# Kernel optimization log

Hardware: AMD Instinct MI355X
Metric: run time of the kernel (lower is better)

The kernel has to match this reference:

```python
import jax, jax.numpy as jnp
import numpy as np

B, N, C = 4, 4096, 1024          # batch, seq_len (input_size), channels
H, D = 16, 64                    # nhead, dim_d (per-head dim)
K_DIM = 256                      # dim_k (Linformer compression)
FF = 4096                        # dim_ff
L = 2                            # depth
EPS = 1e-5


def setup_inputs() -> dict:
    key = jax.random.key(0)
    ks = jax.random.split(key, 16)
    s_qkv = 1.0 / np.sqrt(C)
    s_e = np.sqrt(2.0 / N)        # kaiming_normal fan_in relu
    s_wo = 1.0 / np.sqrt(H * D)
    s_f1 = 1.0 / np.sqrt(C)
    s_f2 = 1.0 / np.sqrt(FF)
    return {
        "x": jax.random.normal(ks[0], (B, N, C), jnp.float32),
        # shared E/F projection (layerwise parameter sharing => one Linear)
        "E_w": jax.random.normal(ks[1], (K_DIM, N), jnp.float32) * s_e,
        "E_b": jax.random.uniform(ks[2], (K_DIM,), jnp.float32, -s_e, s_e),
        # per-layer stacked per-head Q/K/V weights (bias=False)
        "Wq": jax.random.uniform(ks[3], (L, H, D, C), jnp.float32, -s_qkv, s_qkv),
        "Wk": jax.random.uniform(ks[4], (L, H, D, C), jnp.float32, -s_qkv, s_qkv),
        "Wv": jax.random.uniform(ks[5], (L, H, D, C), jnp.float32, -s_qkv, s_qkv),
        "wo_w": jax.random.uniform(ks[6], (L, C, H * D), jnp.float32, -s_wo, s_wo),
        "wo_b": jax.random.uniform(ks[7], (L, C), jnp.float32, -s_wo, s_wo),
        "ln1_g": jnp.ones((L, C), jnp.float32),
        "ln1_b": jnp.zeros((L, C), jnp.float32),
        "ff_w1": jax.random.uniform(ks[8], (L, FF, C), jnp.float32, -s_f1, s_f1),
        "ff_b1": jax.random.uniform(ks[9], (L, FF), jnp.float32, -s_f1, s_f1),
        "ff_w2": jax.random.uniform(ks[10], (L, C, FF), jnp.float32, -s_f2, s_f2),
        "ff_b2": jax.random.uniform(ks[11], (L, C), jnp.float32, -s_f2, s_f2),
        "ln2_g": jnp.ones((L, C), jnp.float32),
        "ln2_b": jnp.zeros((L, C), jnp.float32),
    }


def _layernorm(t, g, b):
    m = jnp.mean(t, axis=-1, keepdims=True)
    v = jnp.var(t, axis=-1, keepdims=True)
    return (t - m) * jax.lax.rsqrt(v + EPS) * g + b


def reference(x, E_w, E_b, Wq, Wk, Wv, wo_w, wo_b, ln1_g, ln1_b,
              ff_w1, ff_b1, ff_w2, ff_b2, ln2_g, ln2_b):
    scale = 1.0 / jnp.sqrt(jnp.float32(D))
    for l in range(Wq.shape[0]):
        # per-head projections, all heads batched: [B,H,N,D]
        Q = jnp.einsum('bnc,hdc->bhnd', x, Wq[l])
        K = jnp.einsum('bnc,hdc->bhnd', x, Wk[l])
        V = jnp.einsum('bnc,hdc->bhnd', x, Wv[l])
        # E-projection of K^T along seq axis: [B,H,D,K_DIM]
        KE = jnp.einsum('bhnd,kn->bhdk', K, E_w) + E_b
        # scores + softmax: [B,H,N,K_DIM]
        P = jax.nn.softmax(jnp.einsum('bhnd,bhdk->bhnk', Q, KE) * scale, axis=-1)
        # F-projection of V (F shares weights with E layerwise): [B,H,K_DIM,D]
        VF = jnp.einsum('bhnd,kn->bhkd', V, E_w) + E_b[:, None]
        attn = jnp.einsum('bhnk,bhkd->bhnd', P, VF)
        # concat heads in head order -> [B,N,H*D]
        cat = jnp.swapaxes(attn, 1, 2).reshape(x.shape[0], x.shape[1], -1)
        out = cat @ wo_w[l].T + wo_b[l]
        x = _layernorm(x + out, ln1_g[l], ln1_b[l])
        # feed-forward (relu)
        h = jax.nn.relu(x @ ff_w1[l].T + ff_b1[l])
        ff = h @ ff_w2[l].T + ff_b2[l]
        x = _layernorm(x + ff, ln2_g[l], ln2_b[l])
    return x
```

## Files before the change

### kernel.cpp

```cpp
#include <hip/hip_runtime.h>
#include <hip/hip_bf16.h>

typedef __attribute__((ext_vector_type(8))) short short8;
typedef __attribute__((ext_vector_type(4))) float f32x4;

__device__ __forceinline__ unsigned short dev_f2bf(float f) {
  __hip_bfloat16 b = __float2bfloat16(f);
  union { __hip_bfloat16 b; unsigned short u; } c; c.b = b; return c.u;
}
__device__ __forceinline__ float dev_bf2f(unsigned short u) {
  union { unsigned int i; float f; } c; c.i = ((unsigned int)u) << 16; return c.f;
}

__device__ __forceinline__ void gload_lds16(const unsigned short* g, unsigned short* l) {
  __builtin_amdgcn_global_load_lds(
      (const __attribute__((address_space(1))) void*)(const void*)g,
      (__attribute__((address_space(3))) void*)(void*)l, 16, 0, 0);
}

struct GemmP {
  const unsigned short* A;
  const unsigned short* B;
  void* C;
  const float* biasN;
  const float* biasM;
  long long aHi, aLo, bHi, bLo, cHi, cLo;
  int K;
  int sAm;
  int sBn;
  int sCm, sCn;
  float scale;
  int relu;
  int cdtype;
};

__global__ __launch_bounds__(512, 2) void gemm256(GemmP p) {
  __shared__ __align__(16) unsigned short lds[2][2][256 * 64];

  const int tid = threadIdx.x;
  const int lane = tid & 63;
  const int wid = tid >> 6;
  const int wm = wid >> 2;
  const int wn = wid & 3;

  int id = blockIdx.y * gridDim.x + blockIdx.x;
  const int nwg = gridDim.x * gridDim.y;
  if ((nwg & 7) == 0) id = (id & 7) * (nwg >> 3) + (id >> 3);
  const long long m0 = (long long)(id / gridDim.y) * 256;
  const long long n0 = (long long)(id % gridDim.y) * 256;

  const int srow8 = lane >> 3;
  const int scol = ((lane & 7) ^ srow8) * 8;

  f32x4 acc[8][4];
#pragma unroll
  for (int i = 0; i < 8; i++)
#pragma unroll
    for (int j = 0; j < 4; j++)
      acc[i][j] = f32x4{0.f, 0.f, 0.f, 0.f};

  const int nt = p.K >> 6;

  auto stage = [&](int buf, int t) {
    const long long k0 = (long long)t * 64;
#pragma unroll
    for (int h = 0; h < 4; h++)
      gload_lds16(p.A + (m0 + h * 64 + wid * 8 + srow8) * p.sAm + k0 + scol,
                  &lds[buf][0][(h * 64 + wid * 8) * 64]);
#pragma unroll
    for (int h = 0; h < 4; h++)
      gload_lds16(p.B + (n0 + h * 64 + wid * 8 + srow8) * p.sBn + k0 + scol,
                  &lds[buf][1][(h * 64 + wid * 8) * 64]);
  };

  stage(0, 0);
  stage(1, 1);

  for (int t = 0; t < nt; t++) {
    const int cur = t & 1;
    if (t + 1 < nt) asm volatile("s_waitcnt vmcnt(8)" ::: "memory");
    else            asm volatile("s_waitcnt vmcnt(0)" ::: "memory");
    __builtin_amdgcn_s_barrier();
    __builtin_amdgcn_sched_barrier(0);

    const unsigned short* Asb = lds[cur][0];
    const unsigned short* Bsb = lds[cur][1];
#pragma unroll
    for (int ks = 0; ks < 2; ks++) {
      const int c16 = ks * 4 + (lane >> 4);
      short8 a[8], b[4];
#pragma unroll
      for (int i = 0; i < 8; i++) {
        const int r = wm * 128 + i * 16 + (lane & 15);
        a[i] = *(const short8*)&Asb[r * 64 + ((c16 ^ (r & 7)) << 3)];
      }
#pragma unroll
      for (int j = 0; j < 4; j++) {
        const int r = wn * 64 + j * 16 + (lane & 15);
        b[j] = *(const short8*)&Bsb[r * 64 + ((c16 ^ (r & 7)) << 3)];
      }
      __builtin_amdgcn_s_setprio(1);
#pragma unroll
      for (int i = 0; i < 8; i++)
#pragma unroll
        for (int j = 0; j < 4; j++)
          acc[i][j] = __builtin_amdgcn_mfma_f32_16x16x32_bf16(a[i], b[j], acc[i][j], 0, 0, 0);
      __builtin_amdgcn_s_setprio(0);
    }
    __builtin_amdgcn_sched_barrier(0);
    __builtin_amdgcn_s_barrier();
    __builtin_amdgcn_sched_barrier(0);
    if (t + 2 < nt) stage(cur, t + 2);
  }

#pragma unroll
  for (int i = 0; i < 8; i++) {
#pragma unroll
    for (int j = 0; j < 4; j++) {
      const int col = (int)n0 + wn * 64 + j * 16 + (lane & 15);
      float bn = p.biasN ? p.biasN[col] : 0.f;
#pragma unroll
      for (int r = 0; r < 4; r++) {
        const long long row = m0 + wm * 128 + i * 16 + ((lane >> 4) << 2) + r;
        float v = acc[i][j][r] * p.scale + bn;
        if (p.relu) v = fmaxf(v, 0.f);
        const long long addr = row * p.sCm + col;
        if (p.cdtype == 0)      ((unsigned short*)p.C)[addr] = dev_f2bf(v);
        else if (p.cdtype == 3) ((float*)p.C)[addr] += v;
        else                    ((float*)p.C)[addr] = v;
      }
    }
  }
}

__global__ __launch_bounds__(256, 2) void attn_kernel(
    const unsigned short* __restrict__ Q, const unsigned short* __restrict__ EK,
    const unsigned short* __restrict__ EVt) {
  __shared__ __align__(16) unsigned short u0[20480];
  __shared__ __align__(16) unsigned short Vs[64 * 256];
  __shared__ float red[2][2][64];

  unsigned short* As = u0;
  unsigned short* Bs = u0 + 4096;
  unsigned short* Ps = u0;

  const int tid = threadIdx.x;
  const int lane = tid & 63;
  const int wid = tid >> 6;
  const int wm = wid >> 1, wn = wid & 1;
  const int m0 = blockIdx.x * 64;
  const int z = blockIdx.z;
  unsigned short* Qz = (unsigned short*)Q + (long long)(z >> 4) * 4194304 + (long long)(z & 15) * 64;
  const unsigned short* EKz = EK + (long long)z * 16384;
  const unsigned short* EVz = EVt + (long long)z * 16384;

  const int srow = tid >> 3;
  const int scol = ((tid & 7) ^ (srow & 7)) * 8;

#pragma unroll
  for (int i = 0; i < 2; i++)
    gload_lds16(Qz + (long long)(m0 + i * 32 + srow) * 1024 + scol, &As[i * 2048 + wid * 512]);
#pragma unroll
  for (int i = 0; i < 8; i++)
    gload_lds16(EKz + (long long)(i * 32 + srow) * 64 + scol, &Bs[i * 2048 + wid * 512]);
#pragma unroll
  for (int c = 0; c < 8; c++) {
    const int pg = (c * 4 + wid) * 64 + lane;
    const int d = pg >> 5, gp = pg & 31;
    gload_lds16(EVz + d * 256 + ((gp ^ (d & 7)) << 3), &Vs[(c * 4 + wid) * 512]);
  }
  __syncthreads();

  f32x4 acc[2][8];
#pragma unroll
  for (int i = 0; i < 2; i++)
#pragma unroll
    for (int j = 0; j < 8; j++)
      acc[i][j] = f32x4{0.f, 0.f, 0.f, 0.f};

#pragma unroll
  for (int ks = 0; ks < 2; ks++) {
    const int c16 = ks * 4 + (lane >> 4);
    short8 a[2], b[8];
#pragma unroll
    for (int i = 0; i < 2; i++) {
      const int row = wm * 32 + i * 16 + (lane & 15);
      a[i] = *(const short8*)&As[row * 64 + ((c16 ^ (row & 7)) << 3)];
    }
#pragma unroll
    for (int j = 0; j < 8; j++) {
      const int row = wn * 128 + j * 16 + (lane & 15);
      b[j] = *(const short8*)&Bs[row * 64 + ((c16 ^ (row & 7)) << 3)];
    }
#pragma unroll
    for (int i = 0; i < 2; i++)
#pragma unroll
      for (int j = 0; j < 8; j++)
        acc[i][j] = __builtin_amdgcn_mfma_f32_16x16x32_bf16(a[i], b[j], acc[i][j], 0, 0, 0);
  }

  const int rr4 = (lane >> 4) << 2;
#pragma unroll
  for (int i = 0; i < 2; i++) {
#pragma unroll
    for (int r = 0; r < 4; r++) {
      float m = acc[i][0][r];
#pragma unroll
      for (int j = 1; j < 8; j++) m = fmaxf(m, acc[i][j][r]);
      m = fmaxf(m, __shfl_xor(m, 1));
      m = fmaxf(m, __shfl_xor(m, 2));
      m = fmaxf(m, __shfl_xor(m, 4));
      m = fmaxf(m, __shfl_xor(m, 8));
      if ((lane & 15) == 0) red[0][wn][wm * 32 + i * 16 + rr4 + r] = m;
    }
  }
  __syncthreads();
  float fm[2][4];
#pragma unroll
  for (int i = 0; i < 2; i++)
#pragma unroll
    for (int r = 0; r < 4; r++) {
      const int row = wm * 32 + i * 16 + rr4 + r;
      fm[i][r] = fmaxf(red[0][0][row], red[0][1][row]);
    }
#pragma unroll
  for (int i = 0; i < 2; i++) {
#pragma unroll
    for (int r = 0; r < 4; r++) {
      float s = 0.f;
#pragma unroll
      for (int j = 0; j < 8; j++) {
        float e = __expf((acc[i][j][r] - fm[i][r]) * 0.125f);
        acc[i][j][r] = e;
        s += e;
      }
      s += __shfl_xor(s, 1);
      s += __shfl_xor(s, 2);
      s += __shfl_xor(s, 4);
      s += __shfl_xor(s, 8);
      if ((lane & 15) == 0) red[1][wn][wm * 32 + i * 16 + rr4 + r] = s;
    }
  }
  __syncthreads();
#pragma unroll
  for (int i = 0; i < 2; i++) {
#pragma unroll
    for (int r = 0; r < 4; r++) {
      const int row = wm * 32 + i * 16 + rr4 + r;
      const float inv = 1.f / (red[1][0][row] + red[1][1][row]);
#pragma unroll
      for (int j = 0; j < 8; j++) {
        const int col = wn * 128 + j * 16 + (lane & 15);
        Ps[row * 256 + (((col >> 3) ^ (row & 7)) << 3) + (col & 7)] =
            dev_f2bf(acc[i][j][r] * inv);
      }
    }
  }
  __syncthreads();

  f32x4 acc2[2][2];
#pragma unroll
  for (int i = 0; i < 2; i++)
#pragma unroll
    for (int jj = 0; jj < 2; jj++)
      acc2[i][jj] = f32x4{0.f, 0.f, 0.f, 0.f};

#pragma unroll
  for (int ks = 0; ks < 8; ks++) {
    const int G = ks * 4 + (lane >> 4);
    short8 pa[2], pb[2];
#pragma unroll
    for (int i = 0; i < 2; i++) {
      const int row = wm * 32 + i * 16 + (lane & 15);
      pa[i] = *(const short8*)&Ps[row * 256 + ((G ^ (row & 7)) << 3)];
    }
#pragma unroll
    for (int jj = 0; jj < 2; jj++) {
      const int d = wn * 32 + jj * 16 + (lane & 15);
      pb[jj] = *(const short8*)&Vs[d * 256 + ((G ^ (d & 7)) << 3)];
    }
#pragma unroll
    for (int i = 0; i < 2; i++)
#pragma unroll
      for (int jj = 0; jj < 2; jj++)
        acc2[i][jj] = __builtin_amdgcn_mfma_f32_16x16x32_bf16(pa[i], pb[jj], acc2[i][jj], 0, 0, 0);
  }

#pragma unroll
  for (int i = 0; i < 2; i++) {
#pragma unroll
    for (int jj = 0; jj < 2; jj++) {
#pragma unroll
      for (int r = 0; r < 4; r++) {
        const int qrow = m0 + wm * 32 + i * 16 + rr4 + r;
        const int dcol = wn * 32 + jj * 16 + (lane & 15);
        Qz[(long long)qrow * 1024 + dcol] = dev_f2bf(acc2[i][jj][r]);
      }
    }
  }
}

template<int BM, int BN, int WM, int WN>
__global__ __launch_bounds__(256, 2) void gemm_nt(GemmP p) {
  constexpr int BK = 64;
  constexpr int TM = BM / WM, TN = BN / WN;
  constexpr int FM = TM / 16, FN = TN / 16;
  __shared__ __align__(16) unsigned short As[BM * BK];
  __shared__ __align__(16) unsigned short Bs[BN * BK];

  const int tid = threadIdx.x;
  const int lane = tid & 63;
  const int wid = tid >> 6;
  const int wm = wid / WN, wn = wid % WN;
  const int m0 = blockIdx.x * BM;
  const int n0 = blockIdx.y * BN;
  const int z = blockIdx.z;
  const int zq = z >> 4, zr = z & 15;
  const unsigned short* Ag = p.A + (long long)zq * p.aHi + (long long)zr * p.aLo;
  const unsigned short* Bg = p.B + (long long)zq * p.bHi + (long long)zr * p.bLo;

  const int srow = tid >> 3;
  const int scol = ((tid & 7) ^ (srow & 7)) * 8;
  constexpr int AC = BM / 32, BC = BN / 32;

  f32x4 acc[FM][FN];
#pragma unroll
  for (int i = 0; i < FM; i++)
#pragma unroll
    for (int j = 0; j < FN; j++)
      acc[i][j] = f32x4{0.f, 0.f, 0.f, 0.f};

  for (int k0 = 0; k0 < p.K; k0 += BK) {
#pragma unroll
    for (int i = 0; i < AC; i++)
      gload_lds16(Ag + (long long)(m0 + i * 32 + srow) * p.sAm + (k0 + scol),
                  &As[i * 2048 + wid * 512]);
#pragma unroll
    for (int i = 0; i < BC; i++)
      gload_lds16(Bg + (long long)(n0 + i * 32 + srow) * p.sBn + (k0 + scol),
                  &Bs[i * 2048 + wid * 512]);
    __syncthreads();
#pragma unroll
    for (int ks = 0; ks < 2; ks++) {
      const int c16 = ks * 4 + (lane >> 4);
      short8 a[FM], b[FN];
#pragma unroll
      for (int i = 0; i < FM; i++) {
        const int row = wm * TM + i * 16 + (lane & 15);
        a[i] = *(const short8*)&As[row * 64 + ((c16 ^ (row & 7)) << 3)];
      }
#pragma unroll
      for (int j = 0; j < FN; j++) {
        const int row = wn * TN + j * 16 + (lane & 15);
        b[j] = *(const short8*)&Bs[row * 64 + ((c16 ^ (row & 7)) << 3)];
      }
#pragma unroll
      for (int i = 0; i < FM; i++)
#pragma unroll
        for (int j = 0; j < FN; j++)
          acc[i][j] = __builtin_amdgcn_mfma_f32_16x16x32_bf16(a[i], b[j], acc[i][j], 0, 0, 0);
    }
    __syncthreads();
  }

  const long long zc_ = (long long)zq * p.cHi + (long long)zr * p.cLo;
#pragma unroll
  for (int i = 0; i < FM; i++) {
#pragma unroll
    for (int j = 0; j < FN; j++) {
      const int col = n0 + wn * TN + j * 16 + (lane & 15);
      float bn = p.biasN ? p.biasN[col] : 0.f;
#pragma unroll
      for (int r = 0; r < 4; r++) {
        const int row = m0 + wm * TM + i * 16 + ((lane >> 4) << 2) + r;
        float v = acc[i][j][r] * p.scale + bn;
        if (p.biasM) v += p.biasM[row];
        if (p.relu) v = fmaxf(v, 0.f);
        const long long addr = zc_ + (long long)row * p.sCm + (long long)col * p.sCn;
        if (p.cdtype == 0)      ((unsigned short*)p.C)[addr] = dev_f2bf(v);
        else if (p.cdtype == 3) ((float*)p.C)[addr] += v;
        else                    ((float*)p.C)[addr] = v;
      }
    }
  }
}

__global__ __launch_bounds__(256) void transpose_kernel(const unsigned short* __restrict__ in,
                                                        unsigned short* __restrict__ out) {
  __shared__ unsigned short t[64][72];
  const int b = blockIdx.z;
  const int n0 = blockIdx.x * 64, c0 = blockIdx.y * 64;
  const int r = threadIdx.x >> 2;
  const int cc = (threadIdx.x & 3) * 16;
  const unsigned short* ip = in + (size_t)b * 4194304 + (size_t)n0 * 1024 + c0;
  *(short8*)&t[r][cc]     = *(const short8*)(ip + (size_t)r * 1024 + cc);
  *(short8*)&t[r][cc + 8] = *(const short8*)(ip + (size_t)r * 1024 + cc + 8);
  __syncthreads();
  unsigned short* op = out + (size_t)b * 4194304 + (size_t)c0 * 4096 + n0;
  short8 w0, w1;
#pragma unroll
  for (int j = 0; j < 8; j++) {
    w0[j] = (short)t[cc + j][r];
    w1[j] = (short)t[cc + 8 + j][r];
  }
  *(short8*)(op + (size_t)r * 4096 + cc)     = w0;
  *(short8*)(op + (size_t)r * 4096 + cc + 8) = w1;
}

__global__ void cvt_kernel(const float* __restrict__ src, unsigned short* __restrict__ dst,
                           float* __restrict__ dstf, long long n4) {
  long long i = (long long)blockIdx.x * blockDim.x + threadIdx.x;
  const long long stride = (long long)gridDim.x * blockDim.x;
  for (; i < n4; i += stride) {
    float4 v = ((const float4*)src)[i];
    ushort4 u;
    u.x = dev_f2bf(v.x); u.y = dev_f2bf(v.y); u.z = dev_f2bf(v.z); u.w = dev_f2bf(v.w);
    ((ushort4*)dst)[i] = u;
    if (dstf) ((float4*)dstf)[i] = v;
  }
}

__global__ __launch_bounds__(256) void add_ln_kernel(float* __restrict__ xf,
    unsigned short* __restrict__ xd,
    const float* __restrict__ g, const float* __restrict__ b, int wx) {
  const long long row = blockIdx.x;
  const int tid = threadIdx.x;
  float4 t = ((const float4*)(xf + row * 1024))[tid];
  ushort4 yv = ((const ushort4*)(xd + row * 1024))[tid];
  t.x += dev_bf2f(yv.x); t.y += dev_bf2f(yv.y);
  t.z += dev_bf2f(yv.z); t.w += dev_bf2f(yv.w);
  float s = t.x + t.y + t.z + t.w;
  float ss = t.x * t.x + t.y * t.y + t.z * t.z + t.w * t.w;
#pragma unroll
  for (int off = 32; off > 0; off >>= 1) { s += __shfl_xor(s, off); ss += __shfl_xor(ss, off); }
  __shared__ float sm[8];
  const int wid = tid >> 6, lane = tid & 63;
  if (lane == 0) { sm[wid] = s; sm[4 + wid] = ss; }
  __syncthreads();
  s = sm[0] + sm[1] + sm[2] + sm[3];
  ss = sm[4] + sm[5] + sm[6] + sm[7];
  const float mean = s * (1.f / 1024.f);
  const float var = ss * (1.f / 1024.f) - mean * mean;
  const float rs = rsqrtf(var + 1e-5f);
  float4 gv = ((const float4*)g)[tid];
  float4 bv = ((const float4*)b)[tid];
  float4 o = {(t.x - mean) * rs * gv.x + bv.x, (t.y - mean) * rs * gv.y + bv.y,
              (t.z - mean) * rs * gv.z + bv.z, (t.w - mean) * rs * gv.w + bv.w};
  ((float4*)(xf + row * 1024))[tid] = o;
  if (wx) {
    ushort4 ob;
    ob.x = dev_f2bf(o.x); ob.y = dev_f2bf(o.y); ob.z = dev_f2bf(o.z); ob.w = dev_f2bf(o.w);
    ((ushort4*)(xd + row * 1024))[tid] = ob;
  }
}

__global__ void fill_canary_kernel(float* p, long long n) {
  long long i = (long long)blockIdx.x * blockDim.x + threadIdx.x;
  const long long stride = (long long)gridDim.x * blockDim.x;
  for (; i < n; i += stride) p[i] = 100.0f;
}

extern "C" void kernel_launch(void* const* d_in, const int* in_sizes, int n_in,
                              void* d_out, int out_size, void* d_ws, size_t ws_size,
                              hipStream_t stream) {
  const float* x_in  = (const float*)d_in[0];
  const float* E_w   = (const float*)d_in[1];
  const float* E_b   = (const float*)d_in[2];
  const float* Wq    = (const float*)d_in[3];
  const float* Wk    = (const float*)d_in[4];
  const float* Wv    = (const float*)d_in[5];
  const float* wo_w  = (const float*)d_in[6];
  const float* wo_b  = (const float*)d_in[7];
  const float* ln1_g = (const float*)d_in[8];
  const float* ln1_b = (const float*)d_in[9];
  const float* ff_w1 = (const float*)d_in[10];
  const float* ff_b1 = (const float*)d_in[11];
  const float* ff_w2 = (const float*)d_in[12];
  const float* ff_b2 = (const float*)d_in[13];
  const float* ln2_g = (const float*)d_in[14];
  const float* ln2_b = (const float*)d_in[15];

  float* xf = (float*)d_out;

  char* ws = (char*)d_ws;
  size_t off = 0;
  auto alloc = [&](size_t bytes) -> char* {
    char* p = ws + off;
    off = (off + bytes + 255) & ~(size_t)255;
    return p;
  };
  unsigned short* E16 = (unsigned short*)alloc(1048576ULL * 2);
  unsigned short* WqL = (unsigned short*)alloc(1048576ULL * 2);
  unsigned short* WkL = (unsigned short*)alloc(1048576ULL * 2);
  unsigned short* WvL = (unsigned short*)alloc(1048576ULL * 2);
  unsigned short* WoL = (unsigned short*)alloc(1048576ULL * 2);
  unsigned short* F1L = (unsigned short*)alloc(4194304ULL * 2);
  unsigned short* F2L = (unsigned short*)alloc(4194304ULL * 2);
  unsigned short* xE  = (unsigned short*)alloc(1048576ULL * 2);
  unsigned short* EK  = (unsigned short*)alloc(1048576ULL * 2);
  unsigned short* EVt = (unsigned short*)alloc(1048576ULL * 2);
  unsigned short* xd  = (unsigned short*)alloc(16777216ULL * 2);
  unsigned short* xT  = (unsigned short*)alloc(16777216ULL * 2);
  unsigned short* Qb4 = xT;

  size_t rem = (ws_size > off) ? ws_size - off : 0;
  size_t Rbytes = rem > 512 ? rem - 512 : 0;
  if (Rbytes > 134217728ULL) Rbytes = 134217728ULL;
  int rowc = 16384;
  while (rowc > 256 && (size_t)rowc * 8192ULL > Rbytes) rowc >>= 1;
  if ((size_t)rowc * 8192ULL > Rbytes) {
    fill_canary_kernel<<<2048, 256, 0, stream>>>(xf, (long long)out_size);
    return;
  }
  char* R = alloc(Rbytes);

  auto cvt = [&](const float* s, unsigned short* d, float* df, long long n) {
    long long n4 = n / 4;
    int grid = (int)((n4 + 255) / 256);
    if (grid > 4096) grid = 4096;
    cvt_kernel<<<grid, 256, 0, stream>>>(s, d, df, n4);
  };

  cvt(x_in, xd, xf, 16777216);
  cvt(E_w, E16, nullptr, 1048576);

  for (int l = 0; l < 2; l++) {
    cvt(Wq + (size_t)l * 1048576, WqL, nullptr, 1048576);
    cvt(Wk + (size_t)l * 1048576, WkL, nullptr, 1048576);
    cvt(Wv + (size_t)l * 1048576, WvL, nullptr, 1048576);
    cvt(wo_w + (size_t)l * 1048576, WoL, nullptr, 1048576);
    cvt(ff_w1 + (size_t)l * 4194304, F1L, nullptr, 4194304);
    cvt(ff_w2 + (size_t)l * 4194304, F2L, nullptr, 4194304);

    transpose_kernel<<<dim3(64, 16, 4), 256, 0, stream>>>(xd, xT);

    GemmP pe{};
    pe.A = E16; pe.sAm = 4096; pe.K = 4096;
    pe.B = xT; pe.sBn = 4096; pe.bLo = 4194304;
    pe.C = xE; pe.cLo = 262144; pe.sCm = 1024; pe.sCn = 1;
    pe.scale = 1.f; pe.cdtype = 0;
    gemm_nt<64,64,2,2><<<dim3(4, 16, 4), 256, 0, stream>>>(pe);

    GemmP pk{};
    pk.A = xE; pk.sAm = 1024; pk.K = 1024; pk.aHi = 262144; pk.aLo = 0;
    pk.B = WkL; pk.sBn = 1024; pk.bHi = 0; pk.bLo = 65536;
    pk.C = EK; pk.cHi = 262144; pk.cLo = 16384; pk.sCm = 64; pk.sCn = 1;
    pk.biasM = E_b; pk.scale = 1.f; pk.cdtype = 0;
    gemm_nt<64,64,2,2><<<dim3(4, 1, 64), 256, 0, stream>>>(pk);
    GemmP pv2 = pk;
    pv2.B = WvL; pv2.C = EVt; pv2.sCm = 1; pv2.sCn = 256;
    gemm_nt<64,64,2,2><<<dim3(4, 1, 64), 256, 0, stream>>>(pv2);

    GemmP pq{};
    pq.A = xd; pq.sAm = 1024; pq.K = 1024;
    pq.B = WqL; pq.sBn = 1024;
    pq.C = Qb4; pq.sCm = 1024; pq.sCn = 1;
    pq.scale = 1.f; pq.cdtype = 0;
    gemm256<<<dim3(64, 4, 1), 512, 0, stream>>>(pq);

    attn_kernel<<<dim3(64, 1, 64), 256, 0, stream>>>(Qb4, EK, EVt);

    GemmP pw{};
    pw.A = Qb4; pw.sAm = 1024; pw.K = 1024;
    pw.B = WoL; pw.sBn = 1024;
    pw.biasN = wo_b + (size_t)l * 1024;
    pw.C = xd; pw.cdtype = 0;
    pw.sCm = 1024; pw.sCn = 1; pw.scale = 1.f;
    gemm256<<<dim3(64, 4, 1), 512, 0, stream>>>(pw);

    add_ln_kernel<<<16384, 256, 0, stream>>>(xf, xd, ln1_g + (size_t)l * 1024,
                                             ln1_b + (size_t)l * 1024, 1);

    for (int r0 = 0; r0 < 16384; r0 += rowc) {
      GemmP f1{};
      f1.A = xd + (size_t)r0 * 1024; f1.sAm = 1024; f1.K = 1024;
      f1.B = F1L; f1.sBn = 1024;
      f1.C = R; f1.sCm = 4096; f1.sCn = 1;
      f1.biasN = ff_b1 + (size_t)l * 4096; f1.scale = 1.f; f1.relu = 1; f1.cdtype = 0;
      gemm256<<<dim3(rowc / 256, 16, 1), 512, 0, stream>>>(f1);

      GemmP f2{};
      f2.A = (unsigned short*)R; f2.sAm = 4096; f2.K = 4096;
      f2.B = F2L; f2.sBn = 4096;
      f2.biasN = ff_b2 + (size_t)l * 1024;
      f2.C = xd + (size_t)r0 * 1024; f2.cdtype = 0;
      f2.sCm = 1024; f2.sCn = 1; f2.scale = 1.f;
      gemm256<<<dim3(rowc / 256, 4, 1), 512, 0, stream>>>(f2);
    }
    add_ln_kernel<<<16384, 256, 0, stream>>>(xf, xd, ln2_g + (size_t)l * 1024,
                                             ln2_b + (size_t)l * 1024, (l == 1) ? 0 : 1);
  }
}
```

Before: 1.320 ms.

## Keep residual stream in bf16 and batch weight conversions before layer loop

```diff
diff --git a/kernel.cpp b/kernel.cpp
--- a/kernel.cpp
+++ b/kernel.cpp
@@ -408,7 +408,7 @@
 }
 
 __global__ void cvt_kernel(const float* __restrict__ src, unsigned short* __restrict__ dst,
-                           float* __restrict__ dstf, long long n4) {
+                           long long n4) {
   long long i = (long long)blockIdx.x * blockDim.x + threadIdx.x;
   const long long stride = (long long)gridDim.x * blockDim.x;
   for (; i < n4; i += stride) {
@@ -416,19 +416,19 @@
     ushort4 u;
     u.x = dev_f2bf(v.x); u.y = dev_f2bf(v.y); u.z = dev_f2bf(v.z); u.w = dev_f2bf(v.w);
     ((ushort4*)dst)[i] = u;
-    if (dstf) ((float4*)dstf)[i] = v;
-  }
-}
-
-__global__ __launch_bounds__(256) void add_ln_kernel(float* __restrict__ xf,
-    unsigned short* __restrict__ xd,
-    const float* __restrict__ g, const float* __restrict__ b, int wx) {
+  }
+}
+
+__global__ __launch_bounds__(256) void add_ln_kernel(
+    const unsigned short* __restrict__ xr, const unsigned short* __restrict__ yr,
+    unsigned short* __restrict__ xw, float* __restrict__ fout,
+    const float* __restrict__ g, const float* __restrict__ b) {
   const long long row = blockIdx.x;
   const int tid = threadIdx.x;
-  float4 t = ((const float4*)(xf + row * 1024))[tid];
-  ushort4 yv = ((const ushort4*)(xd + row * 1024))[tid];
-  t.x += dev_bf2f(yv.x); t.y += dev_bf2f(yv.y);
-  t.z += dev_bf2f(yv.z); t.w += dev_bf2f(yv.w);
+  ushort4 xv = ((const ushort4*)(xr + row * 1024))[tid];
+  ushort4 yv = ((const ushort4*)(yr + row * 1024))[tid];
+  float4 t = {dev_bf2f(xv.x) + dev_bf2f(yv.x), dev_bf2f(xv.y) + dev_bf2f(yv.y),
+              dev_bf2f(xv.z) + dev_bf2f(yv.z), dev_bf2f(xv.w) + dev_bf2f(yv.w)};
   float s = t.x + t.y + t.z + t.w;
   float ss = t.x * t.x + t.y * t.y + t.z * t.z + t.w * t.w;
 #pragma unroll
@@ -446,12 +446,12 @@
   float4 bv = ((const float4*)b)[tid];
   float4 o = {(t.x - mean) * rs * gv.x + bv.x, (t.y - mean) * rs * gv.y + bv.y,
               (t.z - mean) * rs * gv.z + bv.z, (t.w - mean) * rs * gv.w + bv.w};
-  ((float4*)(xf + row * 1024))[tid] = o;
-  if (wx) {
+  if (xw) {
     ushort4 ob;
     ob.x = dev_f2bf(o.x); ob.y = dev_f2bf(o.y); ob.z = dev_f2bf(o.z); ob.w = dev_f2bf(o.w);
-    ((ushort4*)(xd + row * 1024))[tid] = ob;
-  }
+    ((ushort4*)(xw + row * 1024))[tid] = ob;
+  }
+  if (fout) ((float4*)(fout + row * 1024))[tid] = o;
 }
 
 __global__ void fill_canary_kernel(float* p, long long n) {
@@ -480,7 +480,7 @@
   const float* ln2_g = (const float*)d_in[14];
   const float* ln2_b = (const float*)d_in[15];
 
-  float* xf = (float*)d_out;
+  float* xfout = (float*)d_out;
 
   char* ws = (char*)d_ws;
   size_t off = 0;
@@ -490,18 +490,19 @@
     return p;
   };
   unsigned short* E16 = (unsigned short*)alloc(1048576ULL * 2);
-  unsigned short* WqL = (unsigned short*)alloc(1048576ULL * 2);
-  unsigned short* WkL = (unsigned short*)alloc(1048576ULL * 2);
-  unsigned short* WvL = (unsigned short*)alloc(1048576ULL * 2);
-  unsigned short* WoL = (unsigned short*)alloc(1048576ULL * 2);
-  unsigned short* F1L = (unsigned short*)alloc(4194304ULL * 2);
-  unsigned short* F2L = (unsigned short*)alloc(4194304ULL * 2);
+  unsigned short* Wq16 = (unsigned short*)alloc(2097152ULL * 2);
+  unsigned short* Wk16 = (unsigned short*)alloc(2097152ULL * 2);
+  unsigned short* Wv16 = (unsigned short*)alloc(2097152ULL * 2);
+  unsigned short* Wo16 = (unsigned short*)alloc(2097152ULL * 2);
+  unsigned short* F116 = (unsigned short*)alloc(8388608ULL * 2);
+  unsigned short* F216 = (unsigned short*)alloc(8388608ULL * 2);
   unsigned short* xE  = (unsigned short*)alloc(1048576ULL * 2);
   unsigned short* EK  = (unsigned short*)alloc(1048576ULL * 2);
   unsigned short* EVt = (unsigned short*)alloc(1048576ULL * 2);
   unsigned short* xd  = (unsigned short*)alloc(16777216ULL * 2);
   unsigned short* xT  = (unsigned short*)alloc(16777216ULL * 2);
   unsigned short* Qb4 = xT;
+  unsigned short* ybuf = (unsigned short*)alloc(16777216ULL * 2);
 
   size_t rem = (ws_size > off) ? ws_size - off : 0;
   size_t Rbytes = rem > 512 ? rem - 512 : 0;
@@ -509,28 +510,34 @@
   int rowc = 16384;
   while (rowc > 256 && (size_t)rowc * 8192ULL > Rbytes) rowc >>= 1;
   if ((size_t)rowc * 8192ULL > Rbytes) {
-    fill_canary_kernel<<<2048, 256, 0, stream>>>(xf, (long long)out_size);
+    fill_canary_kernel<<<2048, 256, 0, stream>>>(xfout, (long long)out_size);
     return;
   }
   char* R = alloc(Rbytes);
 
-  auto cvt = [&](const float* s, unsigned short* d, float* df, long long n) {
+  auto cvt = [&](const float* s, unsigned short* d, long long n) {
     long long n4 = n / 4;
     int grid = (int)((n4 + 255) / 256);
     if (grid > 4096) grid = 4096;
-    cvt_kernel<<<grid, 256, 0, stream>>>(s, d, df, n4);
+    cvt_kernel<<<grid, 256, 0, stream>>>(s, d, n4);
   };
 
-  cvt(x_in, xd, xf, 16777216);
-  cvt(E_w, E16, nullptr, 1048576);
+  cvt(x_in, xd, 16777216);
+  cvt(E_w, E16, 1048576);
+  cvt(Wq, Wq16, 2097152);
+  cvt(Wk, Wk16, 2097152);
+  cvt(Wv, Wv16, 2097152);
+  cvt(wo_w, Wo16, 2097152);
+  cvt(ff_w1, F116, 8388608);
+  cvt(ff_w2, F216, 8388608);
 
   for (int l = 0; l < 2; l++) {
-    cvt(Wq + (size_t)l * 1048576, WqL, nullptr, 1048576);
-    cvt(Wk + (size_t)l * 1048576, WkL, nullptr, 1048576);
-    cvt(Wv + (size_t)l * 1048576, WvL, nullptr, 1048576);
-    cvt(wo_w + (size_t)l * 1048576, WoL, nullptr, 1048576);
-    cvt(ff_w1 + (size_t)l * 4194304, F1L, nullptr, 4194304);
-    cvt(ff_w2 + (size_t)l * 4194304, F2L, nullptr, 4194304);
+    const unsigned short* WqL = Wq16 + (size_t)l * 1048576;
+    const unsigned short* WkL = Wk16 + (size_t)l * 1048576;
+    const unsigned short* WvL = Wv16 + (size_t)l * 1048576;
+    const unsigned short* WoL = Wo16 + (size_t)l * 1048576;
+    const unsigned short* F1L = F116 + (size_t)l * 4194304;
+    const unsigned short* F2L = F216 + (size_t)l * 4194304;
 
     transpose_kernel<<<dim3(64, 16, 4), 256, 0, stream>>>(xd, xT);
 
@@ -564,12 +571,13 @@
     pw.A = Qb4; pw.sAm = 1024; pw.K = 1024;
     pw.B = WoL; pw.sBn = 1024;
     pw.biasN = wo_b + (size_t)l * 1024;
-    pw.C = xd; pw.cdtype = 0;
+    pw.C = ybuf; pw.cdtype = 0;
     pw.sCm = 1024; pw.sCn = 1; pw.scale = 1.f;
     gemm256<<<dim3(64, 4, 1), 512, 0, stream>>>(pw);
 
-    add_ln_kernel<<<16384, 256, 0, stream>>>(xf, xd, ln1_g + (size_t)l * 1024,
-                                             ln1_b + (size_t)l * 1024, 1);
+    add_ln_kernel<<<16384, 256, 0, stream>>>(xd, ybuf, xd, nullptr,
+                                             ln1_g + (size_t)l * 1024,
+                                             ln1_b + (size_t)l * 1024);
 
     for (int r0 = 0; r0 < 16384; r0 += rowc) {
       GemmP f1{};
@@ -583,11 +591,15 @@
       f2.A = (unsigned short*)R; f2.sAm = 4096; f2.K = 4096;
       f2.B = F2L; f2.sBn = 4096;
       f2.biasN = ff_b2 + (size_t)l * 1024;
-      f2.C = xd + (size_t)r0 * 1024; f2.cdtype = 0;
+      f2.C = ybuf + (size_t)r0 * 1024; f2.cdtype = 0;
       f2.sCm = 1024; f2.sCn = 1; f2.scale = 1.f;
       gemm256<<<dim3(rowc / 256, 4, 1), 512, 0, stream>>>(f2);
     }
-    add_ln_kernel<<<16384, 256, 0, stream>>>(xf, xd, ln2_g + (size_t)l * 1024,
-                                             ln2_b + (size_t)l * 1024, (l == 1) ? 0 : 1);
-  }
-}
+    if (l == 1)
+      add_ln_kernel<<<16384, 256, 0, stream>>>(xd, ybuf, nullptr, xfout,
+                                               ln2_g + 1024, ln2_b + 1024);
+    else
+      add_ln_kernel<<<16384, 256, 0, stream>>>(xd, ybuf, xd, nullptr,
+                                               ln2_g, ln2_b);
+  }
+}
```

Result: slower. 1.440 ms (+9.0%).
